# Optimization experiments

Measured on AMD Instinct MI355X. Metric: run time of the kernel, lower is better.

Reference implementation:

```python
import jax, jax.numpy as jnp
import numpy as np

E, K, H, I = 16, 4, 2048, 1024
B, S = 1, 2048


def setup_inputs() -> dict:
    key = jax.random.key(0)
    ks = jax.random.split(key, 5)
    scale_in = 1.0 / np.sqrt(H)
    scale_mid = 1.0 / np.sqrt(I)
    return {
        "x": jax.random.normal(ks[0], (B, S, H), dtype=jnp.float32),
        "gate_w": jax.random.normal(ks[1], (E, H), dtype=jnp.float32) * scale_in,
        "w1_gate": jax.random.normal(ks[2], (E, I, H), dtype=jnp.float32) * scale_in,
        "w1_up": jax.random.normal(ks[3], (E, I, H), dtype=jnp.float32) * scale_in,
        "w2": jax.random.normal(ks[4], (E, H, I), dtype=jnp.float32) * scale_mid,
        "topk": K,
    }


def reference(x, gate_w, w1_gate, w1_up, w2, topk):
    orig_shape = x.shape
    xt = x.reshape(-1, x.shape[-1])            # [T, H]
    T = xt.shape[0]
    n_exp = gate_w.shape[0]

    # Router: top-k logits, softmax over the selected k (as in the torch code).
    logits = xt @ gate_w.T                      # [T, E]
    topk_vals, topk_ids = jax.lax.top_k(logits, topk)
    topk_w = jax.nn.softmax(topk_vals, axis=-1)  # [T, K]

    # Dense per-token-per-expert combine weight; 0 for unselected experts.
    # Mathematically identical to the gather/scatter-add loop: unselected
    # experts contribute expert_out * 0.
    gate_dense = jnp.zeros((T, n_exp), dtype=xt.dtype)
    gate_dense = gate_dense.at[jnp.arange(T)[:, None], topk_ids].add(topk_w)

    # SwiGLU per expert (dense over experts; weights zero-out unused ones).
    g = jnp.einsum("th,eih->tei", xt, w1_gate)   # [T, E, I]
    u = jnp.einsum("th,eih->tei", xt, w1_up)     # [T, E, I]
    h = jax.nn.silu(g) * u                        # [T, E, I]
    out = jnp.einsum("tei,te,ehi->th", h, gate_dense, w2)  # [T, H]
    return out.reshape(orig_shape)
```

## Files before the change

### kernel.cpp

```cpp
#include <hip/hip_runtime.h>
#include <hip/hip_bf16.h>
#include <stdint.h>

#define NEXP 16
#define KSEL 4
#define HDIM 2048
#define IDIM 1024
#define TTOK 2048
#define NT1 16
#define NTB 16
#define MAXT1 47
#define MAXB1 (MAXT1 * NT1)
#define MAXTB 80
#define MAXBB (MAXTB * NTB)
#define NCVT 1024
#define NCVT1 512
#define NW8 ((NEXP * IDIM * HDIM) / 8)

typedef __attribute__((ext_vector_type(8))) short bf16x8;
typedef __attribute__((ext_vector_type(4))) float f32x4;
typedef unsigned int u32;

__device__ __forceinline__ uint32_t pack2(float a, float b) {
  __hip_bfloat162 h = __float22bfloat162_rn(float2{a, b});
  uint32_t u;
  __builtin_memcpy(&u, &h, 4);
  return u;
}
__device__ __forceinline__ ushort bf1(float a) {
  __hip_bfloat16 h = __float2bfloat16(a);
  ushort u;
  __builtin_memcpy(&u, &h, 2);
  return u;
}
__device__ __forceinline__ void gload16(const void* g, void* l) {
  __builtin_amdgcn_global_load_lds(
      (const __attribute__((address_space(1))) u32*)g,
      (__attribute__((address_space(3))) u32*)l, 16, 0, 0);
}
__device__ __forceinline__ int swzread(int row, int q) {
  return row * 32 + ((q ^ ((row >> 1) & 3)) << 3);
}
__device__ __forceinline__ void cvt_bodyN(const float* __restrict__ src,
                                          ushort* __restrict__ dst,
                                          int idx0, int stride) {
  for (int i = idx0; i < NW8; i += stride) {
    f32x4 a = __builtin_nontemporal_load(((const f32x4*)src) + i * 2);
    f32x4 b = __builtin_nontemporal_load(((const f32x4*)src) + i * 2 + 1);
    uint4 t;
    t.x = pack2(a[0], a[1]); t.y = pack2(a[2], a[3]);
    t.z = pack2(b[0], b[1]); t.w = pack2(b[2], b[3]);
    ((uint4*)dst)[i] = t;
  }
}

__global__ __launch_bounds__(256) void router_kernel(
    const float* __restrict__ x, const float* __restrict__ gw,
    ushort* __restrict__ xb, int* __restrict__ topk_id,
    float* __restrict__ topk_w,
    const float* __restrict__ srcG, ushort* __restrict__ dstG,
    const float* __restrict__ srcU, ushort* __restrict__ dstU)
{
  if (blockIdx.x >= TTOK / 4 + NCVT) {
    cvt_bodyN(srcU, dstU,
              (blockIdx.x - (TTOK / 4 + NCVT)) * 256 + threadIdx.x, NCVT * 256);
    return;
  }
  if (blockIdx.x >= TTOK / 4) {
    cvt_bodyN(srcG, dstG,
              (blockIdx.x - TTOK / 4) * 256 + threadIdx.x, NCVT * 256);
    return;
  }
  const int wid = threadIdx.x >> 6;
  const int lane = threadIdx.x & 63;
  const int t = blockIdx.x * 4 + wid;
  const float4* x4 = (const float4*)(x + (size_t)t * HDIM);
  const float4* gw4 = (const float4*)gw;
  float acc[NEXP];
#pragma unroll
  for (int e = 0; e < NEXP; ++e) acc[e] = 0.f;
#pragma unroll
  for (int i = 0; i < HDIM / 256; ++i) {
    const int idx = i * 64 + lane;
    float4 xv = x4[idx];
    uint2 xp;
    xp.x = pack2(xv.x, xv.y);
    xp.y = pack2(xv.z, xv.w);
    *(uint2*)(xb + (size_t)t * HDIM + idx * 4) = xp;
#pragma unroll
    for (int e = 0; e < NEXP; ++e) {
      float4 wv = gw4[e * (HDIM / 4) + idx];
      acc[e] += xv.x * wv.x + xv.y * wv.y + xv.z * wv.z + xv.w * wv.w;
    }
  }
#pragma unroll
  for (int e = 0; e < NEXP; ++e) {
#pragma unroll
    for (int off = 32; off >= 1; off >>= 1)
      acc[e] += __shfl_xor(acc[e], off);
  }
  if (lane == 0) {
    unsigned taken = 0;
    float vals[KSEL];
    int ids[KSEL];
#pragma unroll
    for (int k = 0; k < KSEL; ++k) {
      float bv = -3.4e38f; int bi = 0;
      for (int e = 0; e < NEXP; ++e)
        if (!((taken >> e) & 1u) && acc[e] > bv) { bv = acc[e]; bi = e; }
      taken |= 1u << bi; vals[k] = bv; ids[k] = bi;
    }
    float m = vals[0], s = 0.f, w[KSEL];
#pragma unroll
    for (int k = 0; k < KSEL; ++k) { w[k] = __expf(vals[k] - m); s += w[k]; }
    float is = 1.f / s;
#pragma unroll
    for (int k = 0; k < KSEL; ++k) {
      topk_id[t * KSEL + k] = ids[k];
      topk_w[t * KSEL + k] = w[k] * is;
    }
  }
}

__global__ __launch_bounds__(1024) void plan_scatter_kernel(
    const int* __restrict__ topk_id, int* __restrict__ counts,
    int* __restrict__ offsets, int* __restrict__ nWA, int* __restrict__ nWB,
    int* __restrict__ wlA, int* __restrict__ wlB,
    int* __restrict__ rowTok, int* __restrict__ inv)
{
  __shared__ int cnt[NEXP], off[NEXP], cur[NEXP];
  __shared__ int t1[NEXP], p1[NEXP], tB[NEXP], pB[NEXP];
  const int tid = threadIdx.x;
  if (tid < NEXP) { cnt[tid] = 0; cur[tid] = 0; }
  __syncthreads();
  for (int i = tid; i < TTOK * KSEL; i += 1024)
    atomicAdd(&cnt[topk_id[i]], 1);
  __syncthreads();
  if (tid == 0) {
    int s = 0, a = 0, b = 0;
    for (int e = 0; e < NEXP; ++e) {
      off[e] = s; s += cnt[e];
      t1[e] = (cnt[e] + 255) >> 8;  p1[e] = a;  a += t1[e];
      tB[e] = (cnt[e] + 127) >> 7;  pB[e] = b;  b += tB[e];
    }
    *nWA = a * NT1;
    *nWB = b * NTB;
  }
  __syncthreads();
  if (tid < NEXP) {
    counts[tid] = cnt[tid];
    offsets[tid] = off[tid];
    const int e = tid, T = t1[e];
    int idx = p1[e] * NT1;
    for (int nt = 0; nt < NT1; ++nt)
      for (int mt = 0; mt < T; ++mt)
        wlA[idx++] = (e << 12) | (nt << 6) | mt;
  } else if (tid < 2 * NEXP) {
    const int e = tid - NEXP, T = tB[e];
    int idx = pB[e] * NTB;
    for (int nt = 0; nt < NTB; ++nt)
      for (int mt = 0; mt < T; ++mt)
        wlB[idx++] = (e << 12) | (nt << 6) | mt;
  }
  for (int i = tid; i < TTOK * KSEL; i += 1024) {
    const int e = topk_id[i];
    const int pos = atomicAdd(&cur[e], 1);
    const int row = off[e] + pos;
    rowTok[row] = i >> 2;
    inv[i] = row;
  }
}

__global__ __launch_bounds__(512) void gemm1_kernel(
    const ushort* __restrict__ xb,
    const ushort* __restrict__ wG, const ushort* __restrict__ wU,
    const int* __restrict__ rowTok, const int* __restrict__ counts,
    const int* __restrict__ offsets, const int* __restrict__ nW,
    const int* __restrict__ wl, ushort* __restrict__ hbuf,
    const float* __restrict__ cvsrc, ushort* __restrict__ cvdst)
{
  if (blockIdx.x >= MAXB1) {
    cvt_bodyN(cvsrc, cvdst,
              (blockIdx.x - MAXB1) * 512 + threadIdx.x, NCVT1 * 512);
    return;
  }
  const int nTot = *nW;
  const int L = (blockIdx.x & 7) * (MAXB1 / 8) + (blockIdx.x >> 3);
  if (L >= nTot) return;
  const int w = wl[L];
  const int e = w >> 12, nt = (w >> 6) & 63, mt = w & 63;
  const int n_e = counts[e], rowbase = offsets[e];

  __shared__ ushort As[2][256 * 32];
  __shared__ ushort Bg[2][64 * 32];
  __shared__ ushort Bu[2][64 * 32];

  const int tid = threadIdx.x;
  const int lane = tid & 63;
  const int wid = tid >> 6;

  const int lr4 = lane >> 2;
  const int ckA = lane & 3;
  const int arl0 = wid * 32 + lr4;
  const int arl1 = wid * 32 + 16 + lr4;
  const int schA0 = (ckA ^ ((arl0 >> 1) & 3)) << 3;
  const int schA1 = (ckA ^ ((arl1 >> 1) & 3)) << 3;
  const int ag0 = mt * 256 + arl0, ag1 = mt * 256 + arl1;
  const int tok0 = rowTok[rowbase + (ag0 < n_e ? ag0 : n_e - 1)];
  const int tok1 = rowTok[rowbase + (ag1 < n_e ? ag1 : n_e - 1)];
  const ushort* pA0 = xb + (size_t)tok0 * HDIM + schA0;
  const ushort* pA1 = xb + (size_t)tok1 * HDIM + schA1;
  const int brl = (wid & 3) * 16 + lr4;
  const int schB = (ckA ^ ((brl >> 1) & 3)) << 3;
  const size_t wbase = (size_t)e * IDIM * HDIM;
  const ushort* pB = ((wid < 4) ? wG : wU) + wbase +
                     (size_t)(nt * 64 + brl) * HDIM + schB;

  const int wr = (wid >> 1) << 6;
  const int wc = (wid & 1) << 5;
  const int lr = lane & 15;
  const int q = lane >> 4;

  f32x4 accG[4][2], accU[4][2];
#pragma unroll
  for (int i = 0; i < 4; ++i)
#pragma unroll
    for (int j = 0; j < 2; ++j) {
      accG[i][j] = (f32x4){0.f, 0.f, 0.f, 0.f};
      accU[i][j] = (f32x4){0.f, 0.f, 0.f, 0.f};
    }

  auto STAGE = [&](int b) {
    gload16(pA0, &As[b][wid * 1024 + lane * 8]);
    gload16(pA1, &As[b][wid * 1024 + 512 + lane * 8]);
    if (wid < 4) gload16(pB, &Bg[b][wid * 512 + lane * 8]);
    else         gload16(pB, &Bu[b][(wid - 4) * 512 + lane * 8]);
    pA0 += 32; pA1 += 32; pB += 32;
  };

  const int NTK = HDIM / 32;
  STAGE(0);
  __syncthreads();
  int buf = 0;
  for (int kt = 0; kt < NTK; ++kt) {
    if (kt + 1 < NTK) STAGE(buf ^ 1);
    bf16x8 af[4], bg[2], bu[2];
#pragma unroll
    for (int mi = 0; mi < 4; ++mi)
      af[mi] = *(const bf16x8*)&As[buf][swzread(wr + mi * 16 + lr, q)];
#pragma unroll
    for (int ni = 0; ni < 2; ++ni) {
      bg[ni] = *(const bf16x8*)&Bg[buf][swzread(wc + ni * 16 + lr, q)];
      bu[ni] = *(const bf16x8*)&Bu[buf][swzread(wc + ni * 16 + lr, q)];
    }
#pragma unroll
    for (int mi = 0; mi < 4; ++mi)
#pragma unroll
      for (int ni = 0; ni < 2; ++ni) {
        accG[mi][ni] = __builtin_amdgcn_mfma_f32_16x16x32_bf16(af[mi], bg[ni], accG[mi][ni], 0, 0, 0);
        accU[mi][ni] = __builtin_amdgcn_mfma_f32_16x16x32_bf16(af[mi], bu[ni], accU[mi][ni], 0, 0, 0);
      }
    __syncthreads();
    buf ^= 1;
  }

#pragma unroll
  for (int mi = 0; mi < 4; ++mi) {
#pragma unroll
    for (int ni = 0; ni < 2; ++ni) {
      const int col = nt * 64 + wc + ni * 16 + lr;
#pragma unroll
      for (int r = 0; r < 4; ++r) {
        const int mrow = mt * 256 + wr + mi * 16 + q * 4 + r;
        if (mrow < n_e) {
          const float gv = accG[mi][ni][r];
          const float uv = accU[mi][ni][r];
          const float hv = (gv / (1.f + __expf(-gv))) * uv;
          hbuf[(size_t)(rowbase + mrow) * IDIM + col] = bf1(hv);
        }
      }
    }
  }
}

__global__ __launch_bounds__(256) void gemmB_kernel(
    const ushort* __restrict__ hb, const ushort* __restrict__ wb,
    const int* __restrict__ counts, const int* __restrict__ offsets,
    const int* __restrict__ nW, const int* __restrict__ wl,
    ushort* __restrict__ po)
{
  const int nTot = *nW;
  const int L = (blockIdx.x & 7) * (MAXBB / 8) + (blockIdx.x >> 3);
  if (L >= nTot) return;
  const int w = wl[L];
  const int e = w >> 12, nt = (w >> 6) & 63, mt = w & 63;
  const int n_e = counts[e], rowbase = offsets[e];

  __shared__ ushort As[2][128 * 32];
  __shared__ ushort Bs[2][128 * 32];

  const int tid = threadIdx.x;
  const int r0 = tid >> 2;
  const int ck = tid & 3;
  const int sch = (ck ^ ((r0 >> 1) & 3)) << 3;

  const int ar0 = mt * 128 + r0, ar1 = ar0 + 64;
  const int g0 = rowbase + (ar0 < n_e ? ar0 : n_e - 1);
  const int g1 = rowbase + (ar1 < n_e ? ar1 : n_e - 1);
  const ushort* pA0 = hb + (size_t)g0 * IDIM + sch;
  const ushort* pA1 = hb + (size_t)g1 * IDIM + sch;
  const size_t wbase = (size_t)e * HDIM * IDIM;
  const ushort* pB0 = wb + wbase + (size_t)(nt * 128 + r0) * IDIM + sch;
  const ushort* pB1 = wb + wbase + (size_t)(nt * 128 + r0 + 64) * IDIM + sch;

  const int lane = tid & 63;
  const int wid = tid >> 6;
  const int wr = (wid >> 1) << 6;
  const int wc = (wid & 1) << 6;
  const int lr = lane & 15;
  const int q = lane >> 4;

  f32x4 acc[4][4];
#pragma unroll
  for (int i = 0; i < 4; ++i)
#pragma unroll
    for (int j = 0; j < 4; ++j) acc[i][j] = (f32x4){0.f, 0.f, 0.f, 0.f};

  auto STAGE = [&](int b) {
    gload16(pA0, &As[b][tid * 8]);
    gload16(pA1, &As[b][2048 + tid * 8]);
    gload16(pB0, &Bs[b][tid * 8]);
    gload16(pB1, &Bs[b][2048 + tid * 8]);
    pA0 += 32; pA1 += 32; pB0 += 32; pB1 += 32;
  };

  const int NTK = IDIM / 32;
  STAGE(0);
  __syncthreads();
  int buf = 0;
  for (int kt = 0; kt < NTK; ++kt) {
    if (kt + 1 < NTK) STAGE(buf ^ 1);
    bf16x8 af[4], bfr[4];
#pragma unroll
    for (int mi = 0; mi < 4; ++mi)
      af[mi] = *(const bf16x8*)&As[buf][swzread(wr + mi * 16 + lr, q)];
#pragma unroll
    for (int ni = 0; ni < 4; ++ni)
      bfr[ni] = *(const bf16x8*)&Bs[buf][swzread(wc + ni * 16 + lr, q)];
#pragma unroll
    for (int mi = 0; mi < 4; ++mi)
#pragma unroll
      for (int ni = 0; ni < 4; ++ni)
        acc[mi][ni] = __builtin_amdgcn_mfma_f32_16x16x32_bf16(af[mi], bfr[ni], acc[mi][ni], 0, 0, 0);
    __syncthreads();
    buf ^= 1;
  }

#pragma unroll
  for (int mi = 0; mi < 4; ++mi) {
#pragma unroll
    for (int ni = 0; ni < 4; ++ni) {
      const int col = nt * 128 + wc + ni * 16 + lr;
#pragma unroll
      for (int r = 0; r < 4; ++r) {
        const int mrow = mt * 128 + wr + mi * 16 + q * 4 + r;
        if (mrow < n_e)
          po[(size_t)(rowbase + mrow) * HDIM + col] = bf1(acc[mi][ni][r]);
      }
    }
  }
}

__global__ __launch_bounds__(256) void combine_kernel(
    const ushort* __restrict__ po, const int* __restrict__ inv,
    const float* __restrict__ tw, float* __restrict__ out)
{
  const int t = blockIdx.x;
  const int r0 = inv[t * 4 + 0], r1 = inv[t * 4 + 1];
  const int r2 = inv[t * 4 + 2], r3 = inv[t * 4 + 3];
  const float w0 = tw[t * 4 + 0], w1 = tw[t * 4 + 1];
  const float w2v = tw[t * 4 + 2], w3 = tw[t * 4 + 3];
  const int i = threadIdx.x;
  uint4 v0 = *(const uint4*)(po + (size_t)r0 * HDIM + i * 8);
  uint4 v1 = *(const uint4*)(po + (size_t)r1 * HDIM + i * 8);
  uint4 v2 = *(const uint4*)(po + (size_t)r2 * HDIM + i * 8);
  uint4 v3 = *(const uint4*)(po + (size_t)r3 * HDIM + i * 8);
  float o[8];
#pragma unroll
  for (int w = 0; w < 4; ++w) {
    const uint32_t a = (&v0.x)[w], b = (&v1.x)[w], c = (&v2.x)[w], d = (&v3.x)[w];
    o[w * 2 + 0] = w0 * __builtin_bit_cast(float, a << 16) +
                   w1 * __builtin_bit_cast(float, b << 16) +
                   w2v * __builtin_bit_cast(float, c << 16) +
                   w3 * __builtin_bit_cast(float, d << 16);
    o[w * 2 + 1] = w0 * __builtin_bit_cast(float, a & 0xffff0000u) +
                   w1 * __builtin_bit_cast(float, b & 0xffff0000u) +
                   w2v * __builtin_bit_cast(float, c & 0xffff0000u) +
                   w3 * __builtin_bit_cast(float, d & 0xffff0000u);
  }
  float4* o4 = (float4*)(out + (size_t)t * HDIM + i * 8);
  o4[0] = (float4){o[0], o[1], o[2], o[3]};
  o4[1] = (float4){o[4], o[5], o[6], o[7]};
}

extern "C" void kernel_launch(void* const* d_in, const int* in_sizes, int n_in,
                              void* d_out, int out_size, void* d_ws, size_t ws_size,
                              hipStream_t stream) {
  const float* x   = (const float*)d_in[0];
  const float* gw  = (const float*)d_in[1];
  const float* w1g = (const float*)d_in[2];
  const float* w1u = (const float*)d_in[3];
  const float* w2  = (const float*)d_in[4];
  float* out = (float*)d_out;

  char* ws = (char*)d_ws;
  ushort* xb    = (ushort*)(ws + 0);
  ushort* wbufG = (ushort*)(ws + 8388608);
  ushort* wbufU = (ushort*)(ws + 75497472);
  ushort* wbuf2 = (ushort*)(ws + 142606336);
  ushort* hbuf  = (ushort*)(ws + 209715200);
  ushort* po    = (ushort*)(ws + 226492416);
  int*    tkid   = (int*)(ws + 260046848);
  float*  tkw    = (float*)(ws + 260046848 + 32768);
  int*    rowTok = (int*)(ws + 260046848 + 65536);
  int*    inv    = (int*)(ws + 260046848 + 98304);
  int*    ctrl   = (int*)(ws + 260177920);
  int* counts  = ctrl;
  int* offsets = ctrl + 32;
  int* nWA     = ctrl + 50;
  int* nWB     = ctrl + 51;
  int* wlA     = ctrl + 64;
  int* wlB     = ctrl + 64 + MAXB1;

  router_kernel<<<TTOK / 4 + 2 * NCVT, 256, 0, stream>>>(
      x, gw, xb, tkid, tkw, w1g, wbufG, w1u, wbufU);
  plan_scatter_kernel<<<1, 1024, 0, stream>>>(tkid, counts, offsets, nWA, nWB,
                                              wlA, wlB, rowTok, inv);
  gemm1_kernel<<<MAXB1 + NCVT1, 512, 0, stream>>>(
      xb, wbufG, wbufU, rowTok, counts, offsets, nWA, wlA, hbuf,
      w2, wbuf2);
  gemmB_kernel<<<MAXBB, 256, 0, stream>>>(hbuf, wbuf2, counts, offsets,
                                          nWB, wlB, po);
  combine_kernel<<<TTOK, 256, 0, stream>>>(po, inv, tkw, out);
}
```

Before: 312.6 us.

## Enlarge down-projection GEMM tile to 256 rows with 512-thread blocks

The second expert GEMM now uses 256x128 output tiles computed by 8 waves instead of 128x128 tiles by 4 waves. The planner reuses the 256-row tile counts from the first GEMM, and the staging loads are reorganised per wave with the same swizzle. Each loaded weight tile is reused across twice as many rows, halving weight traffic and block count. In exchange, the larger A buffer raises LDS use and more rows are wasted on partially filled experts.

```diff
diff --git a/kernel.cpp b/kernel.cpp
--- a/kernel.cpp
+++ b/kernel.cpp
@@ -11,8 +11,7 @@
 #define NTB 16
 #define MAXT1 47
 #define MAXB1 (MAXT1 * NT1)
-#define MAXTB 80
-#define MAXBB (MAXTB * NTB)
+#define MAXBB (MAXT1 * NTB)
 #define NCVT 1024
 #define NCVT1 512
 #define NW8 ((NEXP * IDIM * HDIM) / 8)
@@ -129,7 +128,7 @@
     int* __restrict__ rowTok, int* __restrict__ inv)
 {
   __shared__ int cnt[NEXP], off[NEXP], cur[NEXP];
-  __shared__ int t1[NEXP], p1[NEXP], tB[NEXP], pB[NEXP];
+  __shared__ int t1[NEXP], p1[NEXP];
   const int tid = threadIdx.x;
   if (tid < NEXP) { cnt[tid] = 0; cur[tid] = 0; }
   __syncthreads();
@@ -137,14 +136,13 @@
     atomicAdd(&cnt[topk_id[i]], 1);
   __syncthreads();
   if (tid == 0) {
-    int s = 0, a = 0, b = 0;
+    int s = 0, a = 0;
     for (int e = 0; e < NEXP; ++e) {
       off[e] = s; s += cnt[e];
       t1[e] = (cnt[e] + 255) >> 8;  p1[e] = a;  a += t1[e];
-      tB[e] = (cnt[e] + 127) >> 7;  pB[e] = b;  b += tB[e];
     }
     *nWA = a * NT1;
-    *nWB = b * NTB;
+    *nWB = a * NTB;
   }
   __syncthreads();
   if (tid < NEXP) {
@@ -156,8 +154,8 @@
       for (int mt = 0; mt < T; ++mt)
         wlA[idx++] = (e << 12) | (nt << 6) | mt;
   } else if (tid < 2 * NEXP) {
-    const int e = tid - NEXP, T = tB[e];
-    int idx = pB[e] * NTB;
+    const int e = tid - NEXP, T = t1[e];
+    int idx = p1[e] * NTB;
     for (int nt = 0; nt < NTB; ++nt)
       for (int mt = 0; mt < T; ++mt)
         wlB[idx++] = (e << 12) | (nt << 6) | mt;
@@ -283,7 +281,7 @@
   }
 }
 
-__global__ __launch_bounds__(256) void gemmB_kernel(
+__global__ __launch_bounds__(512) void gemmB_kernel(
     const ushort* __restrict__ hb, const ushort* __restrict__ wb,
     const int* __restrict__ counts, const int* __restrict__ offsets,
     const int* __restrict__ nW, const int* __restrict__ wl,
@@ -296,25 +294,29 @@
   const int e = w >> 12, nt = (w >> 6) & 63, mt = w & 63;
   const int n_e = counts[e], rowbase = offsets[e];
 
-  __shared__ ushort As[2][128 * 32];
+  __shared__ ushort As[2][256 * 32];
   __shared__ ushort Bs[2][128 * 32];
 
   const int tid = threadIdx.x;
-  const int r0 = tid >> 2;
-  const int ck = tid & 3;
-  const int sch = (ck ^ ((r0 >> 1) & 3)) << 3;
-
-  const int ar0 = mt * 128 + r0, ar1 = ar0 + 64;
-  const int g0 = rowbase + (ar0 < n_e ? ar0 : n_e - 1);
-  const int g1 = rowbase + (ar1 < n_e ? ar1 : n_e - 1);
-  const ushort* pA0 = hb + (size_t)g0 * IDIM + sch;
-  const ushort* pA1 = hb + (size_t)g1 * IDIM + sch;
-  const size_t wbase = (size_t)e * HDIM * IDIM;
-  const ushort* pB0 = wb + wbase + (size_t)(nt * 128 + r0) * IDIM + sch;
-  const ushort* pB1 = wb + wbase + (size_t)(nt * 128 + r0 + 64) * IDIM + sch;
-
   const int lane = tid & 63;
   const int wid = tid >> 6;
+
+  const int lr4 = lane >> 2;
+  const int ckA = lane & 3;
+  const int arl0 = wid * 32 + lr4;
+  const int arl1 = wid * 32 + 16 + lr4;
+  const int schA0 = (ckA ^ ((arl0 >> 1) & 3)) << 3;
+  const int schA1 = (ckA ^ ((arl1 >> 1) & 3)) << 3;
+  const int ag0 = mt * 256 + arl0, ag1 = mt * 256 + arl1;
+  const int g0 = rowbase + (ag0 < n_e ? ag0 : n_e - 1);
+  const int g1 = rowbase + (ag1 < n_e ? ag1 : n_e - 1);
+  const ushort* pA0 = hb + (size_t)g0 * IDIM + schA0;
+  const ushort* pA1 = hb + (size_t)g1 * IDIM + schA1;
+  const int brl = wid * 16 + lr4;
+  const int schB = (ckA ^ ((brl >> 1) & 3)) << 3;
+  const size_t wbase = (size_t)e * HDIM * IDIM;
+  const ushort* pB = wb + wbase + (size_t)(nt * 128 + brl) * IDIM + schB;
+
   const int wr = (wid >> 1) << 6;
   const int wc = (wid & 1) << 6;
   const int lr = lane & 15;
@@ -327,11 +329,10 @@
     for (int j = 0; j < 4; ++j) acc[i][j] = (f32x4){0.f, 0.f, 0.f, 0.f};
 
   auto STAGE = [&](int b) {
-    gload16(pA0, &As[b][tid * 8]);
-    gload16(pA1, &As[b][2048 + tid * 8]);
-    gload16(pB0, &Bs[b][tid * 8]);
-    gload16(pB1, &Bs[b][2048 + tid * 8]);
-    pA0 += 32; pA1 += 32; pB0 += 32; pB1 += 32;
+    gload16(pA0, &As[b][wid * 1024 + lane * 8]);
+    gload16(pA1, &As[b][wid * 1024 + 512 + lane * 8]);
+    gload16(pB, &Bs[b][wid * 512 + lane * 8]);
+    pA0 += 32; pA1 += 32; pB += 32;
   };
 
   const int NTK = IDIM / 32;
@@ -363,7 +364,7 @@
       const int col = nt * 128 + wc + ni * 16 + lr;
 #pragma unroll
       for (int r = 0; r < 4; ++r) {
-        const int mrow = mt * 128 + wr + mi * 16 + q * 4 + r;
+        const int mrow = mt * 256 + wr + mi * 16 + q * 4 + r;
         if (mrow < n_e)
           po[(size_t)(rowbase + mrow) * HDIM + col] = bf1(acc[mi][ni][r]);
       }
@@ -439,7 +440,7 @@
   gemm1_kernel<<<MAXB1 + NCVT1, 512, 0, stream>>>(
       xb, wbufG, wbufU, rowTok, counts, offsets, nWA, wlA, hbuf,
       w2, wbuf2);
-  gemmB_kernel<<<MAXBB, 256, 0, stream>>>(hbuf, wbuf2, counts, offsets,
+  gemmB_kernel<<<MAXBB, 512, 0, stream>>>(hbuf, wbuf2, counts, offsets,
                                           nWB, wlB, po);
   combine_kernel<<<TTOK, 256, 0, stream>>>(po, inv, tkw, out);
 }
```

Result: no change. 310.2 us (-0.8%).
